# Performance work log

Hardware: AMD Instinct MI355X
Metric: run time of the kernel (lower is better)

## Reference

```python
import jax, jax.numpy as jnp
import numpy as np

EPS = 1e-10
W_SILOG, W_L2, W_BINS = 1.0, 1.0, 1.0  # w_masked=1.0 -> invalid branch skipped


def setup_inputs() -> dict:
    key = jax.random.key(0)
    k1, k2, k3, k4 = jax.random.split(key, 4)
    B, H, W = 8, 240, 320
    NB = 256  # n_bins
    prediction = jax.random.uniform(k1, (B, 1, H, W), dtype=jnp.float32)
    target = jax.random.uniform(k2, (B, 1, H, W), dtype=jnp.float32)
    bin_edges = jax.random.uniform(k3, (B, NB + 1), dtype=jnp.float32)
    mask = jax.random.randint(k4, (B, 1, H, W), 0, 2).astype(jnp.bool_)
    return {"prediction": prediction, "target": target, "bin_edges": bin_edges, "mask": mask}


def _onedirectional_dist(a, b):
    # a: [B, Na], b: [B, Nb] -> sum over Na of min_j (a_i - b_j)^2, shape [B]
    d2 = (a[:, :, None] - b[:, None, :]) ** 2  # [B, Na, Nb]
    return jnp.min(d2, axis=2).sum(axis=1)


def reference(prediction, target, bin_edges, mask):
    # Chamfer distance between bin centers and target depth values
    bin_centers = 0.5 * (bin_edges[:, :-1] + bin_edges[:, 1:])  # [B, NB]
    target_depths = target.reshape(target.shape[0], -1)         # [B, H*W]
    chamfer = (_onedirectional_dist(bin_centers, target_depths)
               + _onedirectional_dist(target_depths, bin_centers)).mean()

    # Masked reductions (equivalent to boolean-indexed means, jit-friendly)
    p = prediction.reshape(-1)
    t = target.reshape(-1)
    fm = mask.reshape(-1).astype(p.dtype)
    cnt = fm.sum()

    # L2: sqrt(MSE over masked elements)
    l2 = jnp.sqrt(jnp.sum((p - t) ** 2 * fm) / cnt)

    # SILog
    d = jnp.log(p + EPS) - jnp.log(t + EPS)
    d_mean = jnp.sum(d * fm) / cnt
    d2_mean = jnp.sum(d * d * fm) / cnt
    silog = 10.0 * jnp.sqrt(d2_mean - 0.85 * d_mean ** 2)

    return W_L2 * l2 + W_SILOG * silog + W_BINS * chamfer
```

## Files before the change

kernel.cpp:

```cpp
#include <hip/hip_runtime.h>
#include <math.h>

#define NPIX   614400
#define HW     76800
#define NBATCH 8
#define NB     256
#define NEDGE  257
#define ELEMS  4
#define MAIN_BLOCKS (NPIX / (256 * ELEMS))
#define BPB (MAIN_BLOCKS / NBATCH)
#define DET_BYTES 16384
#define FINF 3.402823466e+38f


__device__ __forceinline__ double wsum64(double v) {
#pragma unroll
  for (int o = 32; o > 0; o >>= 1) v += __shfl_down(v, o, 64);
  return v;
}

__global__ void k_prep(const float* __restrict__ edges,
                       const unsigned char* __restrict__ mask,
                       double* __restrict__ sums,
                       unsigned int* __restrict__ flag,
                       float* __restrict__ cs,
                       unsigned int* __restrict__ gD) {
  const int tid = threadIdx.x;
  const int b = blockIdx.x;
  if (b < NBATCH) {
    __shared__ float s[NB];
    float v = 0.5f * (edges[b * NEDGE + tid] + edges[b * NEDGE + tid + 1]);
    for (int k = 2; k <= NB; k <<= 1) {
      for (int j = k >> 1; j > 0; j >>= 1) {
        float partner;
        if (j < 64) {
          partner = __shfl_xor(v, j, 64);
        } else {
          s[tid] = v;
          __syncthreads();
          partner = s[tid ^ j];
          __syncthreads();
        }
        const bool up = ((tid & k) == 0);
        const bool lowhalf = ((tid & j) == 0);
        v = (lowhalf == up) ? fminf(v, partner) : fmaxf(v, partner);
      }
    }
    cs[b * NB + tid] = v;
    gD[b * NB + tid] = 0x7F800000u;
  } else {
    unsigned int c = 0;
    for (int i = tid; i < DET_BYTES; i += 256) c += (mask[i] != 0) ? 1u : 0u;
#pragma unroll
    for (int o = 32; o > 0; o >>= 1) c += __shfl_down(c, o, 64);
    __shared__ unsigned int sh[4];
    if ((tid & 63) == 0) sh[tid >> 6] = c;
    __syncthreads();
    if (tid == 0) *flag = ((sh[0] + sh[1] + sh[2] + sh[3]) > (DET_BYTES / 4)) ? 1u : 0u;
    if (tid < 5) sums[tid] = 0.0;
  }
}

__global__ void k_main(const float* __restrict__ p, const float* __restrict__ t,
                       const void* __restrict__ mask,
                       const unsigned int* __restrict__ flag,
                       const float* __restrict__ cs,
                       double* __restrict__ sums,
                       unsigned int* __restrict__ gD) {
  __shared__ float c_lds[NB];
  __shared__ unsigned int d_lds[NB];
  __shared__ double shred[4][5];
  const int tid = threadIdx.x;
  const int b = blockIdx.x / BPB;
  const int base = blockIdx.x * (256 * ELEMS) + tid * ELEMS;

  c_lds[tid] = cs[b * NB + tid];
  d_lds[tid] = 0x7F800000u;
  __syncthreads();

  const float4 p4 = *(const float4*)(p + base);
  const float4 t4 = *(const float4*)(t + base);
  float pe[ELEMS] = {p4.x, p4.y, p4.z, p4.w};
  float te[ELEMS] = {t4.x, t4.y, t4.z, t4.w};
  int me[ELEMS];
  if (*flag) {
    uchar4 m4 = *(const uchar4*)((const unsigned char*)mask + base);
    me[0] = m4.x; me[1] = m4.y; me[2] = m4.z; me[3] = m4.w;
  } else {
    int4 m4 = *(const int4*)((const int*)mask + base);
    me[0] = m4.x; me[1] = m4.y; me[2] = m4.z; me[3] = m4.w;
  }

  double cnt = 0, ssq = 0, sd = 0, sd2 = 0, dir2 = 0;
#pragma unroll
  for (int e = 0; e < ELEMS; ++e) {
    const float pi = pe[e], ti = te[e];
    if (me[e]) {
      float diff = pi - ti;
      float d = logf(pi + 1e-10f) - logf(ti + 1e-10f);
      cnt += 1.0;
      ssq += (double)diff * (double)diff;
      sd  += (double)d;
      sd2 += (double)d * (double)d;
    }
    int k = -1;
#pragma unroll
    for (int s = 128; s > 0; s >>= 1) {
      int nk = k + s;
      if (nk < NB && c_lds[nk] <= ti) k = nk;
    }
    float dl = (k >= 0)     ? ti - c_lds[k]     : 1e30f;
    float dr = (k + 1 < NB) ? c_lds[k + 1] - ti : 1e30f;
    if (k >= 0)     atomicMin(&d_lds[k],     __float_as_uint(dl));
    if (k + 1 < NB) atomicMin(&d_lds[k + 1], __float_as_uint(dr));
    float dmin = fminf(dl, dr);
    dir2 += (double)dmin * (double)dmin;
  }

  __syncthreads();
  atomicMin(&gD[b * NB + tid], d_lds[tid]);

  double v[5] = {cnt, ssq, sd, sd2, dir2};
  const int lane = tid & 63, wid = tid >> 6;
#pragma unroll
  for (int i = 0; i < 5; ++i) {
    double r = wsum64(v[i]);
    if (lane == 0) shred[wid][i] = r;
  }
  __syncthreads();
  if (tid < 5) {
    double r = shred[0][tid] + shred[1][tid] + shred[2][tid] + shred[3][tid];
    atomicAdd(&sums[tid], r);
  }
}

__global__ void k_final(const double* __restrict__ sums,
                        const float* __restrict__ cs,
                        const unsigned int* __restrict__ gD,
                        float* __restrict__ out) {
  __shared__ double shred[4];
  const int tid = threadIdx.x;
  const int lane = tid & 63, wid = tid >> 6;
  double dir1 = 0.0;

#pragma unroll
  for (int r = 0; r < 2; ++r) {
    const int b = wid + r * 4;
    const float4 c4 = *(const float4*)(cs + b * NB + lane * 4);
    const uint4 d4 = *(const uint4*)(gD + b * NB + lane * 4);
    float c[4] = {c4.x, c4.y, c4.z, c4.w};
    float D[4] = {__uint_as_float(d4.x), __uint_as_float(d4.y),
                  __uint_as_float(d4.z), __uint_as_float(d4.w)};

    float pa[4];
    pa[0] = D[0] - c[0];
    pa[1] = fminf(pa[0], D[1] - c[1]);
    pa[2] = fminf(pa[1], D[2] - c[2]);
    pa[3] = fminf(pa[2], D[3] - c[3]);
    float s = pa[3];
#pragma unroll
    for (int off = 1; off < 64; off <<= 1) {
      float u = __shfl_up(s, off, 64);
      if (lane >= off) s = fminf(s, u);
    }
    float exL = __shfl_up(s, 1, 64);
    if (lane == 0) exL = FINF;

    float sb[4];
    sb[3] = D[3] + c[3];
    sb[2] = fminf(sb[3], D[2] + c[2]);
    sb[1] = fminf(sb[2], D[1] + c[1]);
    sb[0] = fminf(sb[1], D[0] + c[0]);
    float s2 = sb[0];
#pragma unroll
    for (int off = 1; off < 64; off <<= 1) {
      float u = __shfl_down(s2, off, 64);
      if (lane + off < 64) s2 = fminf(s2, u);
    }
    float exR = __shfl_down(s2, 1, 64);
    if (lane == 63) exR = FINF;

#pragma unroll
    for (int i = 0; i < 4; ++i) {
      float pref = fminf(exL, pa[i]);
      float suf  = fminf(exR, sb[i]);
      float dist = fminf(pref + c[i], suf - c[i]);
      dir1 += (double)dist * (double)dist;
    }
  }

  dir1 = wsum64(dir1);
  if (lane == 0) shred[wid] = dir1;
  __syncthreads();
  if (tid == 0) {
    double d1 = shred[0] + shred[1] + shred[2] + shred[3];
    double cnt = sums[0], ssq = sums[1], sd = sums[2], sd2 = sums[3], d2 = sums[4];
    double l2 = sqrt(ssq / cnt);
    double dm = sd / cnt, d2m = sd2 / cnt;
    double silog = 10.0 * sqrt(d2m - 0.85 * dm * dm);
    double chamfer = (d1 + d2) / (double)NBATCH;
    out[0] = (float)(l2 + silog + chamfer);
  }
}

extern "C" void kernel_launch(void* const* d_in, const int* in_sizes, int n_in,
                              void* d_out, int out_size, void* d_ws, size_t ws_size,
                              hipStream_t stream) {
  const float* pred  = (const float*)d_in[0];
  const float* targ  = (const float*)d_in[1];
  const float* edges = (const float*)d_in[2];
  const void*  mask  = d_in[3];

  char* ws = (char*)d_ws;
  double* sums       = (double*)ws;
  unsigned int* flag = (unsigned int*)(ws + 48);
  float* cs          = (float*)(ws + 64);
  unsigned int* gD   = (unsigned int*)(ws + 8256);

  k_prep<<<NBATCH + 1, NB, 0, stream>>>(edges, (const unsigned char*)mask,
                                        sums, flag, cs, gD);
  k_main<<<MAIN_BLOCKS, NB, 0, stream>>>(pred, targ, mask, flag, cs, sums, gD);
  k_final<<<1, NB, 0, stream>>>(sums, cs, gD, (float*)d_out);
}
```

Baseline: 25.41 us.

## Fuse prep, main and final kernels into one with last-block ticket finalization

Merges the three launches into one kernel. Every block now sorts its own batch's bin centers redundantly and detects the mask format itself, and the last block to arrive, chosen by an atomic ticket, runs the final chamfer and loss reduction. Workspace initialization moves to a hipMemsetAsync, with the min-distance buffer encoded as an inverted atomicMax so a zero fill is a valid neutral value. This removes two kernel launches and their inter-kernel gaps, at the cost of a redundant per-block bitonic sort and extra barriers, plus a memset node.

```diff
diff --git a/kernel.cpp b/kernel.cpp
--- a/kernel.cpp
+++ b/kernel.cpp
@@ -9,7 +9,6 @@
 #define ELEMS  4
 #define MAIN_BLOCKS (NPIX / (256 * ELEMS))
 #define BPB (MAIN_BLOCKS / NBATCH)
-#define DET_BYTES 16384
 #define FINF 3.402823466e+38f
 
 
@@ -19,71 +18,65 @@
   return v;
 }
 
-__global__ void k_prep(const float* __restrict__ edges,
-                       const unsigned char* __restrict__ mask,
-                       double* __restrict__ sums,
-                       unsigned int* __restrict__ flag,
-                       float* __restrict__ cs,
-                       unsigned int* __restrict__ gD) {
-  const int tid = threadIdx.x;
-  const int b = blockIdx.x;
-  if (b < NBATCH) {
-    __shared__ float s[NB];
-    float v = 0.5f * (edges[b * NEDGE + tid] + edges[b * NEDGE + tid + 1]);
-    for (int k = 2; k <= NB; k <<= 1) {
-      for (int j = k >> 1; j > 0; j >>= 1) {
-        float partner;
-        if (j < 64) {
-          partner = __shfl_xor(v, j, 64);
-        } else {
-          s[tid] = v;
-          __syncthreads();
-          partner = s[tid ^ j];
-          __syncthreads();
-        }
-        const bool up = ((tid & k) == 0);
-        const bool lowhalf = ((tid & j) == 0);
-        v = (lowhalf == up) ? fminf(v, partner) : fmaxf(v, partner);
-      }
-    }
-    cs[b * NB + tid] = v;
-    gD[b * NB + tid] = 0x7F800000u;
-  } else {
-    unsigned int c = 0;
-    for (int i = tid; i < DET_BYTES; i += 256) c += (mask[i] != 0) ? 1u : 0u;
-#pragma unroll
-    for (int o = 32; o > 0; o >>= 1) c += __shfl_down(c, o, 64);
-    __shared__ unsigned int sh[4];
-    if ((tid & 63) == 0) sh[tid >> 6] = c;
-    __syncthreads();
-    if (tid == 0) *flag = ((sh[0] + sh[1] + sh[2] + sh[3]) > (DET_BYTES / 4)) ? 1u : 0u;
-    if (tid < 5) sums[tid] = 0.0;
-  }
-}
-
-__global__ void k_main(const float* __restrict__ p, const float* __restrict__ t,
-                       const void* __restrict__ mask,
-                       const unsigned int* __restrict__ flag,
-                       const float* __restrict__ cs,
-                       double* __restrict__ sums,
-                       unsigned int* __restrict__ gD) {
+__device__ __forceinline__ unsigned int nzb(unsigned int w) {
+  return ((w & 0xFFu) != 0u) + (((w >> 8) & 0xFFu) != 0u) +
+         (((w >> 16) & 0xFFu) != 0u) + ((w >> 24) != 0u);
+}
+
+__global__ void __launch_bounds__(256) k_fused(
+    const float* __restrict__ p, const float* __restrict__ t,
+    const void* __restrict__ mask, const float* __restrict__ edges,
+    double* __restrict__ sums, unsigned int* __restrict__ ticket,
+    unsigned int* __restrict__ gD, float* __restrict__ cs,
+    float* __restrict__ out) {
   __shared__ float c_lds[NB];
   __shared__ unsigned int d_lds[NB];
   __shared__ double shred[4][5];
+  __shared__ unsigned int sh_u[4];
+  __shared__ unsigned int last_flag;
+
   const int tid = threadIdx.x;
+  const int lane = tid & 63, wid = tid >> 6;
   const int b = blockIdx.x / BPB;
   const int base = blockIdx.x * (256 * ELEMS) + tid * ELEMS;
 
-  c_lds[tid] = cs[b * NB + tid];
-  d_lds[tid] = 0x7F800000u;
-  __syncthreads();
-
   const float4 p4 = *(const float4*)(p + base);
   const float4 t4 = *(const float4*)(t + base);
+
+  uint4 raw = ((const uint4*)mask)[tid];
+  unsigned int cnz = nzb(raw.x) + nzb(raw.y) + nzb(raw.z) + nzb(raw.w);
+#pragma unroll
+  for (int o = 32; o > 0; o >>= 1) cnz += __shfl_down(cnz, o, 64);
+  if (lane == 0) sh_u[wid] = cnz;
+  __syncthreads();
+  const bool bytemode = (sh_u[0] + sh_u[1] + sh_u[2] + sh_u[3]) > 1024u;
+
+  float v = 0.5f * (edges[b * NEDGE + tid] + edges[b * NEDGE + tid + 1]);
+  for (int k = 2; k <= NB; k <<= 1) {
+    for (int j = k >> 1; j > 0; j >>= 1) {
+      float partner;
+      if (j < 64) {
+        partner = __shfl_xor(v, j, 64);
+      } else {
+        __syncthreads();
+        c_lds[tid] = v;
+        __syncthreads();
+        partner = c_lds[tid ^ j];
+      }
+      const bool up = ((tid & k) == 0);
+      const bool low = ((tid & j) == 0);
+      v = (low == up) ? fminf(v, partner) : fmaxf(v, partner);
+    }
+  }
+  __syncthreads();
+  c_lds[tid] = v;
+  d_lds[tid] = 0u;
+  __syncthreads();
+
   float pe[ELEMS] = {p4.x, p4.y, p4.z, p4.w};
   float te[ELEMS] = {t4.x, t4.y, t4.z, t4.w};
   int me[ELEMS];
-  if (*flag) {
+  if (bytemode) {
     uchar4 m4 = *(const uchar4*)((const unsigned char*)mask + base);
     me[0] = m4.x; me[1] = m4.y; me[2] = m4.z; me[3] = m4.w;
   } else {
@@ -111,59 +104,66 @@
     }
     float dl = (k >= 0)     ? ti - c_lds[k]     : 1e30f;
     float dr = (k + 1 < NB) ? c_lds[k + 1] - ti : 1e30f;
-    if (k >= 0)     atomicMin(&d_lds[k],     __float_as_uint(dl));
-    if (k + 1 < NB) atomicMin(&d_lds[k + 1], __float_as_uint(dr));
+    if (k >= 0)     atomicMax(&d_lds[k],     ~__float_as_uint(dl));
+    if (k + 1 < NB) atomicMax(&d_lds[k + 1], ~__float_as_uint(dr));
     float dmin = fminf(dl, dr);
     dir2 += (double)dmin * (double)dmin;
   }
 
   __syncthreads();
-  atomicMin(&gD[b * NB + tid], d_lds[tid]);
-
-  double v[5] = {cnt, ssq, sd, sd2, dir2};
-  const int lane = tid & 63, wid = tid >> 6;
+  {
+    unsigned int dv = d_lds[tid];
+    if (dv) atomicMax(&gD[b * NB + tid], dv);
+  }
+  if ((blockIdx.x % BPB) == 0) {
+    atomicExch(&cs[b * NB + tid], c_lds[tid]);
+  }
+
+  double acc[5] = {cnt, ssq, sd, sd2, dir2};
 #pragma unroll
   for (int i = 0; i < 5; ++i) {
-    double r = wsum64(v[i]);
+    double r = wsum64(acc[i]);
     if (lane == 0) shred[wid][i] = r;
   }
   __syncthreads();
   if (tid < 5) {
-    double r = shred[0][tid] + shred[1][tid] + shred[2][tid] + shred[3][tid];
-    atomicAdd(&sums[tid], r);
-  }
-}
-
-__global__ void k_final(const double* __restrict__ sums,
-                        const float* __restrict__ cs,
-                        const unsigned int* __restrict__ gD,
-                        float* __restrict__ out) {
-  __shared__ double shred[4];
-  const int tid = threadIdx.x;
-  const int lane = tid & 63, wid = tid >> 6;
+    atomicAdd(&sums[tid],
+              shred[0][tid] + shred[1][tid] + shred[2][tid] + shred[3][tid]);
+  }
+
+  __threadfence();
+  __syncthreads();
+  if (tid == 0)
+    last_flag = (atomicAdd(ticket, 1u) == (unsigned)(MAIN_BLOCKS - 1)) ? 1u : 0u;
+  __syncthreads();
+  if (last_flag == 0u) return;
+  __threadfence();
+
   double dir1 = 0.0;
-
 #pragma unroll
   for (int r = 0; r < 2; ++r) {
-    const int b = wid + r * 4;
-    const float4 c4 = *(const float4*)(cs + b * NB + lane * 4);
-    const uint4 d4 = *(const uint4*)(gD + b * NB + lane * 4);
-    float c[4] = {c4.x, c4.y, c4.z, c4.w};
-    float D[4] = {__uint_as_float(d4.x), __uint_as_float(d4.y),
-                  __uint_as_float(d4.z), __uint_as_float(d4.w)};
+    const int bb = wid + r * 4;
+    float c[4], D[4];
+#pragma unroll
+    for (int i = 0; i < 4; ++i) {
+      const int idx = bb * NB + lane * 4 + i;
+      c[i] = __uint_as_float(atomicOr((unsigned int*)&cs[idx], 0u));
+      unsigned int s = atomicOr(&gD[idx], 0u);
+      D[i] = s ? __uint_as_float(~s) : FINF;
+    }
 
     float pa[4];
     pa[0] = D[0] - c[0];
     pa[1] = fminf(pa[0], D[1] - c[1]);
     pa[2] = fminf(pa[1], D[2] - c[2]);
     pa[3] = fminf(pa[2], D[3] - c[3]);
-    float s = pa[3];
+    float s1 = pa[3];
 #pragma unroll
     for (int off = 1; off < 64; off <<= 1) {
-      float u = __shfl_up(s, off, 64);
-      if (lane >= off) s = fminf(s, u);
-    }
-    float exL = __shfl_up(s, 1, 64);
+      float u = __shfl_up(s1, off, 64);
+      if (lane >= off) s1 = fminf(s1, u);
+    }
+    float exL = __shfl_up(s1, 1, 64);
     if (lane == 0) exL = FINF;
 
     float sb[4];
@@ -190,15 +190,19 @@
   }
 
   dir1 = wsum64(dir1);
-  if (lane == 0) shred[wid] = dir1;
+  if (lane == 0) shred[wid][0] = dir1;
   __syncthreads();
   if (tid == 0) {
-    double d1 = shred[0] + shred[1] + shred[2] + shred[3];
-    double cnt = sums[0], ssq = sums[1], sd = sums[2], sd2 = sums[3], d2 = sums[4];
-    double l2 = sqrt(ssq / cnt);
-    double dm = sd / cnt, d2m = sd2 / cnt;
+    double d1 = shred[0][0] + shred[1][0] + shred[2][0] + shred[3][0];
+    double cnt_ = atomicAdd(&sums[0], 0.0);
+    double ssq_ = atomicAdd(&sums[1], 0.0);
+    double sd_  = atomicAdd(&sums[2], 0.0);
+    double sd2_ = atomicAdd(&sums[3], 0.0);
+    double d2_  = atomicAdd(&sums[4], 0.0);
+    double l2 = sqrt(ssq_ / cnt_);
+    double dm = sd_ / cnt_, d2m = sd2_ / cnt_;
     double silog = 10.0 * sqrt(d2m - 0.85 * dm * dm);
-    double chamfer = (d1 + d2) / (double)NBATCH;
+    double chamfer = (d1 + d2_) / (double)NBATCH;
     out[0] = (float)(l2 + silog + chamfer);
   }
 }
@@ -212,13 +216,12 @@
   const void*  mask  = d_in[3];
 
   char* ws = (char*)d_ws;
-  double* sums       = (double*)ws;
-  unsigned int* flag = (unsigned int*)(ws + 48);
-  float* cs          = (float*)(ws + 64);
-  unsigned int* gD   = (unsigned int*)(ws + 8256);
-
-  k_prep<<<NBATCH + 1, NB, 0, stream>>>(edges, (const unsigned char*)mask,
-                                        sums, flag, cs, gD);
-  k_main<<<MAIN_BLOCKS, NB, 0, stream>>>(pred, targ, mask, flag, cs, sums, gD);
-  k_final<<<1, NB, 0, stream>>>(sums, cs, gD, (float*)d_out);
-}
+  double* sums         = (double*)ws;
+  unsigned int* ticket = (unsigned int*)(ws + 40);
+  unsigned int* gD     = (unsigned int*)(ws + 64);
+  float* cs            = (float*)(ws + 8256);
+
+  hipMemsetAsync(ws, 0, 8256, stream);
+  k_fused<<<MAIN_BLOCKS, NB, 0, stream>>>(pred, targ, mask, edges,
+                                          sums, ticket, gD, cs, (float*)d_out);
+}
```

Result: slower. 55.68 us (+119.2%).
